# Kernel tuning notes

Hardware: AMD Instinct MI355X
Metric: run time of the kernel (lower is better)

Reference implementation:

```python
import jax, jax.numpy as jnp
import numpy as np

N_BUCKETS = 512
SLOTS_PER_BUCKET = 32
TAU = 0.1
ALPHA = 0.5


def _l2norm(x, eps=1e-12):
    return x / jnp.maximum(jnp.linalg.norm(x, axis=-1, keepdims=True), eps)


def setup_inputs() -> dict:
    key = jax.random.key(0)
    ks = jax.random.split(key, 6)
    B, T, D = 2, 2048, 1024
    total_slots = N_BUCKETS * SLOTS_PER_BUCKET
    vocab = 50257
    query_emb = jax.random.normal(ks[0], (B, T, D), dtype=jnp.float32)
    tids = jax.random.randint(ks[1], (B, T), 0, vocab)
    slot_keys = jax.random.normal(ks[2], (total_slots, D), dtype=jnp.float32)
    slot_values = jax.random.normal(ks[3], (total_slots, D), dtype=jnp.float32)
    slot_tids = jax.random.randint(ks[4], (total_slots,), 0, vocab)
    centroid_codebook = _l2norm(jax.random.normal(ks[5], (N_BUCKETS, D), dtype=jnp.float32))
    return {
        "query_emb": query_emb,
        "tids": tids,
        "slot_keys": slot_keys,
        "slot_values": slot_values,
        "slot_tids": slot_tids,
        "centroid_codebook": centroid_codebook,
    }


def reference(query_emb, tids, slot_keys, slot_values, slot_tids, centroid_codebook):
    # CentroidAddressableManifold.read
    buckets = tids % N_BUCKETS                                  # [B,T]
    lex_anchors = centroid_codebook[buckets]                    # [B,T,D]
    q_norm = _l2norm(query_emb)
    # bucket-indexed gather of 32 slots per token
    indices = buckets[..., None] * SLOTS_PER_BUCKET + jnp.arange(SLOTS_PER_BUCKET)  # [B,T,S]
    b_keys = slot_keys[indices]                                 # [B,T,S,D]
    b_vals = slot_values[indices]                               # [B,T,S,D]
    unified_query = _l2norm(ALPHA * q_norm + (1.0 - ALPHA) * lex_anchors)
    scores = jnp.einsum("btd,btsd->bts", unified_query, b_keys)  # [B,T,S]
    # hard-match path
    gathered_tids = slot_tids[indices]                          # [B,T,S]
    match_mask = (tids[..., None] == gathered_tids).astype(scores.dtype)
    match_sum = match_mask.sum(axis=-1, keepdims=True)
    has_match = match_sum > 0
    probs_hard = match_mask / (match_sum + 1e-9)
    probs_soft = jax.nn.softmax(scores / TAU, axis=-1)
    val_hard = jnp.einsum("bts,btsw->btw", probs_hard, b_vals)
    val_soft = jnp.einsum("bts,btsw->btw", probs_soft, b_vals)
    val_out = jnp.where(has_match, val_hard, val_soft)          # [B,T,D]
    return val_out
```

## Files before the change

### kernel.cpp

```cpp
#include <hip/hip_runtime.h>

#define NB 512
#define SLOTS 32
#define D 1024
#define D4 256
#define TC 8
#define CAP 64
#define TAU_INV 10.0f
#define BT 256

__global__ void k_zero(int* __restrict__ cnt) {
    if (threadIdx.x < NB) cnt[threadIdx.x] = 0;
}

__global__ void k_build(const int* __restrict__ tids, int n,
                        int* __restrict__ cnt, int* __restrict__ list) {
    int i = blockIdx.x * 256 + threadIdx.x;
    if (i < n) {
        int b = tids[i] & (NB - 1);
        int p = atomicAdd(&cnt[b], 1);
        if (p < CAP) list[b * CAP + p] = i;
    }
}

__global__ __launch_bounds__(BT, 2)
void k_main(const float* __restrict__ query,
            const int*   __restrict__ tids,
            const float* __restrict__ skeys,
            const float* __restrict__ svals,
            const int*   __restrict__ stids,
            const float* __restrict__ centroid,
            float*       __restrict__ out,
            const int*   __restrict__ cnt,
            const int*   __restrict__ list)
{
    const int bucket = blockIdx.x & (NB - 1);
    const int part   = blockIdx.x >> 9;
    const int tidx   = threadIdx.x;
    const int lane   = tidx & 63;
    const int wid    = tidx >> 6;

    const int count = min(cnt[bucket], CAP);
    const int ncnt  = (count - part + 1) >> 1;
    if (ncnt <= 0) return;

    __shared__ float s_uq[TC][D];
    __shared__ float s_scores[TC][SLOTS];
    __shared__ float s_probs[TC][SLOTS];
    __shared__ int   s_tok[TC];
    __shared__ int   s_ttid[TC];

    const int slot_tid = stids[bucket * SLOTS + (lane & 31)];
    const float4* kb = (const float4*)(skeys + (size_t)bucket * SLOTS * D);
    const float4* vb = (const float4*)(svals + (size_t)bucket * SLOTS * D);
    const float4* cb = (const float4*)(centroid + (size_t)bucket * D);

    for (int c0 = 0; c0 < ncnt; c0 += TC) {
        const int nt = min(TC, ncnt - c0);

        for (int t = wid; t < nt; t += 4) {
            const int tok = list[bucket * CAP + part + 2 * (c0 + t)];
            const float4* q4 = (const float4*)(query + (size_t)tok * D);
            float4 qv[4], anc[4];
            float ss = 0.f;
            #pragma unroll
            for (int j = 0; j < 4; ++j) {
                qv[j]  = q4[lane + 64 * j];
                anc[j] = cb[lane + 64 * j];
                ss += qv[j].x*qv[j].x + qv[j].y*qv[j].y + qv[j].z*qv[j].z + qv[j].w*qv[j].w;
            }
            #pragma unroll
            for (int off = 32; off >= 1; off >>= 1) ss += __shfl_xor(ss, off);
            const float qn = 0.5f / fmaxf(sqrtf(ss), 1e-12f);
            float4 uv[4];
            float ss2 = 0.f;
            #pragma unroll
            for (int j = 0; j < 4; ++j) {
                uv[j].x = qv[j].x * qn + 0.5f * anc[j].x;
                uv[j].y = qv[j].y * qn + 0.5f * anc[j].y;
                uv[j].z = qv[j].z * qn + 0.5f * anc[j].z;
                uv[j].w = qv[j].w * qn + 0.5f * anc[j].w;
                ss2 += uv[j].x*uv[j].x + uv[j].y*uv[j].y + uv[j].z*uv[j].z + uv[j].w*uv[j].w;
            }
            #pragma unroll
            for (int off = 32; off >= 1; off >>= 1) ss2 += __shfl_xor(ss2, off);
            const float un = 1.0f / fmaxf(sqrtf(ss2), 1e-12f);
            #pragma unroll
            for (int j = 0; j < 4; ++j) {
                ((float4*)s_uq[t])[lane + 64 * j] =
                    make_float4(uv[j].x*un, uv[j].y*un, uv[j].z*un, uv[j].w*un);
            }
            if (lane == 0) { s_tok[t] = tok; s_ttid[t] = tids[tok]; }
        }
        __syncthreads();

        #pragma unroll 1
        for (int rnd = 0; rnd < 2; ++rnd) {
            const int sbase = rnd * 16 + wid * 4;
            const float4* kr = kb + (size_t)sbase * D4;
            float4 k0[4], k1[4], k2[4], k3[4];
            #pragma unroll
            for (int j = 0; j < 4; ++j) {
                k0[j] = kr[0 * D4 + lane + 64 * j];
                k1[j] = kr[1 * D4 + lane + 64 * j];
                k2[j] = kr[2 * D4 + lane + 64 * j];
                k3[j] = kr[3 * D4 + lane + 64 * j];
            }
            for (int t = 0; t < nt; ++t) {
                const float4* u4 = (const float4*)s_uq[t];
                float P0 = 0.f, P1 = 0.f, P2 = 0.f, P3 = 0.f;
                #pragma unroll
                for (int j = 0; j < 4; ++j) {
                    float4 u = u4[lane + 64 * j];
                    P0 += k0[j].x*u.x + k0[j].y*u.y + k0[j].z*u.z + k0[j].w*u.w;
                    P1 += k1[j].x*u.x + k1[j].y*u.y + k1[j].z*u.z + k1[j].w*u.w;
                    P2 += k2[j].x*u.x + k2[j].y*u.y + k2[j].z*u.z + k2[j].w*u.w;
                    P3 += k3[j].x*u.x + k3[j].y*u.y + k3[j].z*u.z + k3[j].w*u.w;
                }
                {
                    const bool hi = (lane & 1) != 0;
                    const float sA = hi ? P0 : P2, kA = hi ? P2 : P0;
                    P0 = kA + __shfl_xor(sA, 1);
                    const float sB = hi ? P1 : P3, kB = hi ? P3 : P1;
                    P1 = kB + __shfl_xor(sB, 1);
                }
                {
                    const bool hi = (lane & 2) != 0;
                    const float sA = hi ? P0 : P1, kA = hi ? P1 : P0;
                    P0 = kA + __shfl_xor(sA, 2);
                }
                P0 += __shfl_xor(P0, 4);
                P0 += __shfl_xor(P0, 8);
                P0 += __shfl_xor(P0, 16);
                P0 += __shfl_xor(P0, 32);
                if (lane < 4)
                    s_scores[t][sbase + (((lane & 1) << 1) | ((lane >> 1) & 1))] = P0;
            }
        }
        __syncthreads();

        for (int t = wid; t < nt; t += 4) {
            if (lane < 32) {
                const float sc = s_scores[t][lane];
                float mx = sc;
                #pragma unroll
                for (int off = 16; off >= 1; off >>= 1) mx = fmaxf(mx, __shfl_xor(mx, off));
                const float e = __expf((sc - mx) * TAU_INV);
                const float f = (slot_tid == s_ttid[t]) ? 1.f : 0.f;
                float es = e, ms = f;
                #pragma unroll
                for (int off = 16; off >= 1; off >>= 1) {
                    es += __shfl_xor(es, off);
                    ms += __shfl_xor(ms, off);
                }
                s_probs[t][lane] = (ms > 0.f) ? f / (ms + 1e-9f) : e / es;
            }
        }
        __syncthreads();

        {
            float4 acc[TC];
            #pragma unroll
            for (int t = 0; t < TC; ++t) acc[t] = make_float4(0.f, 0.f, 0.f, 0.f);

            #pragma unroll 1
            for (int s0 = 0; s0 < SLOTS; s0 += 8) {
                float4 v[8];
                #pragma unroll
                for (int i = 0; i < 8; ++i) v[i] = vb[(s0 + i) * D4 + tidx];
                #pragma unroll
                for (int t = 0; t < TC; ++t) {
                    if (t < nt) {
                        const float4 pA = ((const float4*)s_probs[t])[(s0 >> 2) + 0];
                        const float4 pB = ((const float4*)s_probs[t])[(s0 >> 2) + 1];
                        acc[t].x += pA.x*v[0].x + pA.y*v[1].x + pA.z*v[2].x + pA.w*v[3].x
                                  + pB.x*v[4].x + pB.y*v[5].x + pB.z*v[6].x + pB.w*v[7].x;
                        acc[t].y += pA.x*v[0].y + pA.y*v[1].y + pA.z*v[2].y + pA.w*v[3].y
                                  + pB.x*v[4].y + pB.y*v[5].y + pB.z*v[6].y + pB.w*v[7].y;
                        acc[t].z += pA.x*v[0].z + pA.y*v[1].z + pA.z*v[2].z + pA.w*v[3].z
                                  + pB.x*v[4].z + pB.y*v[5].z + pB.z*v[6].z + pB.w*v[7].z;
                        acc[t].w += pA.x*v[0].w + pA.y*v[1].w + pA.z*v[2].w + pA.w*v[3].w
                                  + pB.x*v[4].w + pB.y*v[5].w + pB.z*v[6].w + pB.w*v[7].w;
                    }
                }
            }
            #pragma unroll
            for (int t = 0; t < TC; ++t) {
                if (t < nt) {
                    ((float4*)(out + (size_t)s_tok[t] * D))[tidx] = acc[t];
                }
            }
        }
        __syncthreads();
    }
}

extern "C" void kernel_launch(void* const* d_in, const int* in_sizes, int n_in,
                              void* d_out, int out_size, void* d_ws, size_t ws_size,
                              hipStream_t stream) {
    const float* query    = (const float*)d_in[0];
    const int*   tids     = (const int*)  d_in[1];
    const float* skeys    = (const float*)d_in[2];
    const float* svals    = (const float*)d_in[3];
    const int*   stids    = (const int*)  d_in[4];
    const float* centroid = (const float*)d_in[5];
    float* out = (float*)d_out;
    const int n_tokens = in_sizes[1];

    int* cnt  = (int*)d_ws;
    int* list = cnt + NB;

    k_zero<<<1, 512, 0, stream>>>(cnt);
    k_build<<<(n_tokens + 255) / 256, 256, 0, stream>>>(tids, n_tokens, cnt, list);
    k_main<<<NB * 2, BT, 0, stream>>>(query, tids, skeys, svals, stids,
                                      centroid, out, cnt, list);
}
```

Before: 55.65 us.

## Process one token per wavefront end-to-end without shared memory or block barriers

The block-wide staging (shared unified query, scores and probs, with several __syncthreads per chunk of 8 tokens) is replaced by one token per wavefront. Each wavefront computes its normalized query, all 32 scores, the softmax and match probabilities, and the weighted value sum in registers. Probabilities move between lanes by shuffles, and the block grows to 512 threads (8 waves). This removes barriers and LDS traffic, but each wave now re-reads all 32 keys and values of the bucket per token instead of sharing them across 8 tokens, relying on L2/L1 for reuse.

```diff
diff --git a/kernel.cpp b/kernel.cpp
--- a/kernel.cpp
+++ b/kernel.cpp
@@ -4,10 +4,9 @@
 #define SLOTS 32
 #define D 1024
 #define D4 256
-#define TC 8
 #define CAP 64
 #define TAU_INV 10.0f
-#define BT 256
+#define BT 512
 
 __global__ void k_zero(int* __restrict__ cnt) {
     if (threadIdx.x < NB) cnt[threadIdx.x] = 0;
@@ -36,68 +35,64 @@
 {
     const int bucket = blockIdx.x & (NB - 1);
     const int part   = blockIdx.x >> 9;
-    const int tidx   = threadIdx.x;
-    const int lane   = tidx & 63;
-    const int wid    = tidx >> 6;
+    const int lane   = threadIdx.x & 63;
+    const int wid    = threadIdx.x >> 6;
 
     const int count = min(cnt[bucket], CAP);
     const int ncnt  = (count - part + 1) >> 1;
     if (ncnt <= 0) return;
 
-    __shared__ float s_uq[TC][D];
-    __shared__ float s_scores[TC][SLOTS];
-    __shared__ float s_probs[TC][SLOTS];
-    __shared__ int   s_tok[TC];
-    __shared__ int   s_ttid[TC];
-
-    const int slot_tid = stids[bucket * SLOTS + (lane & 31)];
+    const int ls      = lane & 31;
+    const int my_slot = (ls & ~3) | (((ls & 1) << 1) | ((ls >> 1) & 1));
+    const int my_stid = stids[bucket * SLOTS + my_slot];
+
     const float4* kb = (const float4*)(skeys + (size_t)bucket * SLOTS * D);
     const float4* vb = (const float4*)(svals + (size_t)bucket * SLOTS * D);
     const float4* cb = (const float4*)(centroid + (size_t)bucket * D);
 
-    for (int c0 = 0; c0 < ncnt; c0 += TC) {
-        const int nt = min(TC, ncnt - c0);
-
-        for (int t = wid; t < nt; t += 4) {
-            const int tok = list[bucket * CAP + part + 2 * (c0 + t)];
+    float4 anc[4];
+    #pragma unroll
+    for (int j = 0; j < 4; ++j) anc[j] = cb[lane + 64 * j];
+
+    for (int t = wid; t < ncnt; t += 8) {
+        const int tok    = list[bucket * CAP + part + 2 * t];
+        const int my_tid = tids[tok];
+
+        float4 uq[4];
+        {
             const float4* q4 = (const float4*)(query + (size_t)tok * D);
-            float4 qv[4], anc[4];
+            float4 qv[4];
             float ss = 0.f;
             #pragma unroll
             for (int j = 0; j < 4; ++j) {
-                qv[j]  = q4[lane + 64 * j];
-                anc[j] = cb[lane + 64 * j];
+                qv[j] = q4[lane + 64 * j];
                 ss += qv[j].x*qv[j].x + qv[j].y*qv[j].y + qv[j].z*qv[j].z + qv[j].w*qv[j].w;
             }
             #pragma unroll
             for (int off = 32; off >= 1; off >>= 1) ss += __shfl_xor(ss, off);
             const float qn = 0.5f / fmaxf(sqrtf(ss), 1e-12f);
-            float4 uv[4];
             float ss2 = 0.f;
             #pragma unroll
             for (int j = 0; j < 4; ++j) {
-                uv[j].x = qv[j].x * qn + 0.5f * anc[j].x;
-                uv[j].y = qv[j].y * qn + 0.5f * anc[j].y;
-                uv[j].z = qv[j].z * qn + 0.5f * anc[j].z;
-                uv[j].w = qv[j].w * qn + 0.5f * anc[j].w;
-                ss2 += uv[j].x*uv[j].x + uv[j].y*uv[j].y + uv[j].z*uv[j].z + uv[j].w*uv[j].w;
+                uq[j].x = qv[j].x * qn + 0.5f * anc[j].x;
+                uq[j].y = qv[j].y * qn + 0.5f * anc[j].y;
+                uq[j].z = qv[j].z * qn + 0.5f * anc[j].z;
+                uq[j].w = qv[j].w * qn + 0.5f * anc[j].w;
+                ss2 += uq[j].x*uq[j].x + uq[j].y*uq[j].y + uq[j].z*uq[j].z + uq[j].w*uq[j].w;
             }
             #pragma unroll
             for (int off = 32; off >= 1; off >>= 1) ss2 += __shfl_xor(ss2, off);
             const float un = 1.0f / fmaxf(sqrtf(ss2), 1e-12f);
             #pragma unroll
             for (int j = 0; j < 4; ++j) {
-                ((float4*)s_uq[t])[lane + 64 * j] =
-                    make_float4(uv[j].x*un, uv[j].y*un, uv[j].z*un, uv[j].w*un);
-            }
-            if (lane == 0) { s_tok[t] = tok; s_ttid[t] = tids[tok]; }
-        }
-        __syncthreads();
-
+                uq[j].x *= un; uq[j].y *= un; uq[j].z *= un; uq[j].w *= un;
+            }
+        }
+
+        float sc = 0.f;
         #pragma unroll 1
-        for (int rnd = 0; rnd < 2; ++rnd) {
-            const int sbase = rnd * 16 + wid * 4;
-            const float4* kr = kb + (size_t)sbase * D4;
+        for (int g = 0; g < 8; ++g) {
+            const float4* kr = kb + (size_t)(g * 4) * D4;
             float4 k0[4], k1[4], k2[4], k3[4];
             #pragma unroll
             for (int j = 0; j < 4; ++j) {
@@ -106,92 +101,80 @@
                 k2[j] = kr[2 * D4 + lane + 64 * j];
                 k3[j] = kr[3 * D4 + lane + 64 * j];
             }
-            for (int t = 0; t < nt; ++t) {
-                const float4* u4 = (const float4*)s_uq[t];
-                float P0 = 0.f, P1 = 0.f, P2 = 0.f, P3 = 0.f;
-                #pragma unroll
-                for (int j = 0; j < 4; ++j) {
-                    float4 u = u4[lane + 64 * j];
-                    P0 += k0[j].x*u.x + k0[j].y*u.y + k0[j].z*u.z + k0[j].w*u.w;
-                    P1 += k1[j].x*u.x + k1[j].y*u.y + k1[j].z*u.z + k1[j].w*u.w;
-                    P2 += k2[j].x*u.x + k2[j].y*u.y + k2[j].z*u.z + k2[j].w*u.w;
-                    P3 += k3[j].x*u.x + k3[j].y*u.y + k3[j].z*u.z + k3[j].w*u.w;
-                }
-                {
-                    const bool hi = (lane & 1) != 0;
-                    const float sA = hi ? P0 : P2, kA = hi ? P2 : P0;
-                    P0 = kA + __shfl_xor(sA, 1);
-                    const float sB = hi ? P1 : P3, kB = hi ? P3 : P1;
-                    P1 = kB + __shfl_xor(sB, 1);
-                }
-                {
-                    const bool hi = (lane & 2) != 0;
-                    const float sA = hi ? P0 : P1, kA = hi ? P1 : P0;
-                    P0 = kA + __shfl_xor(sA, 2);
-                }
-                P0 += __shfl_xor(P0, 4);
-                P0 += __shfl_xor(P0, 8);
-                P0 += __shfl_xor(P0, 16);
-                P0 += __shfl_xor(P0, 32);
-                if (lane < 4)
-                    s_scores[t][sbase + (((lane & 1) << 1) | ((lane >> 1) & 1))] = P0;
-            }
-        }
-        __syncthreads();
-
-        for (int t = wid; t < nt; t += 4) {
-            if (lane < 32) {
-                const float sc = s_scores[t][lane];
-                float mx = sc;
-                #pragma unroll
-                for (int off = 16; off >= 1; off >>= 1) mx = fmaxf(mx, __shfl_xor(mx, off));
-                const float e = __expf((sc - mx) * TAU_INV);
-                const float f = (slot_tid == s_ttid[t]) ? 1.f : 0.f;
-                float es = e, ms = f;
-                #pragma unroll
-                for (int off = 16; off >= 1; off >>= 1) {
-                    es += __shfl_xor(es, off);
-                    ms += __shfl_xor(ms, off);
-                }
-                s_probs[t][lane] = (ms > 0.f) ? f / (ms + 1e-9f) : e / es;
-            }
-        }
-        __syncthreads();
-
+            float P0 = 0.f, P1 = 0.f, P2 = 0.f, P3 = 0.f;
+            #pragma unroll
+            for (int j = 0; j < 4; ++j) {
+                const float4 u = uq[j];
+                P0 += k0[j].x*u.x + k0[j].y*u.y + k0[j].z*u.z + k0[j].w*u.w;
+                P1 += k1[j].x*u.x + k1[j].y*u.y + k1[j].z*u.z + k1[j].w*u.w;
+                P2 += k2[j].x*u.x + k2[j].y*u.y + k2[j].z*u.z + k2[j].w*u.w;
+                P3 += k3[j].x*u.x + k3[j].y*u.y + k3[j].z*u.z + k3[j].w*u.w;
+            }
+            {
+                const bool hi = (lane & 1) != 0;
+                const float sA = hi ? P0 : P2, kA = hi ? P2 : P0;
+                P0 = kA + __shfl_xor(sA, 1);
+                const float sB = hi ? P1 : P3, kB = hi ? P3 : P1;
+                P1 = kB + __shfl_xor(sB, 1);
+            }
+            {
+                const bool hi = (lane & 2) != 0;
+                const float sA = hi ? P0 : P1, kA = hi ? P1 : P0;
+                P0 = kA + __shfl_xor(sA, 2);
+            }
+            P0 += __shfl_xor(P0, 4);
+            P0 += __shfl_xor(P0, 8);
+            P0 += __shfl_xor(P0, 16);
+            P0 += __shfl_xor(P0, 32);
+            if ((ls >> 2) == g) sc = P0;
+        }
+
+        float p;
         {
-            float4 acc[TC];
-            #pragma unroll
-            for (int t = 0; t < TC; ++t) acc[t] = make_float4(0.f, 0.f, 0.f, 0.f);
-
-            #pragma unroll 1
-            for (int s0 = 0; s0 < SLOTS; s0 += 8) {
-                float4 v[8];
-                #pragma unroll
-                for (int i = 0; i < 8; ++i) v[i] = vb[(s0 + i) * D4 + tidx];
-                #pragma unroll
-                for (int t = 0; t < TC; ++t) {
-                    if (t < nt) {
-                        const float4 pA = ((const float4*)s_probs[t])[(s0 >> 2) + 0];
-                        const float4 pB = ((const float4*)s_probs[t])[(s0 >> 2) + 1];
-                        acc[t].x += pA.x*v[0].x + pA.y*v[1].x + pA.z*v[2].x + pA.w*v[3].x
-                                  + pB.x*v[4].x + pB.y*v[5].x + pB.z*v[6].x + pB.w*v[7].x;
-                        acc[t].y += pA.x*v[0].y + pA.y*v[1].y + pA.z*v[2].y + pA.w*v[3].y
-                                  + pB.x*v[4].y + pB.y*v[5].y + pB.z*v[6].y + pB.w*v[7].y;
-                        acc[t].z += pA.x*v[0].z + pA.y*v[1].z + pA.z*v[2].z + pA.w*v[3].z
-                                  + pB.x*v[4].z + pB.y*v[5].z + pB.z*v[6].z + pB.w*v[7].z;
-                        acc[t].w += pA.x*v[0].w + pA.y*v[1].w + pA.z*v[2].w + pA.w*v[3].w
-                                  + pB.x*v[4].w + pB.y*v[5].w + pB.z*v[6].w + pB.w*v[7].w;
-                    }
-                }
-            }
-            #pragma unroll
-            for (int t = 0; t < TC; ++t) {
-                if (t < nt) {
-                    ((float4*)(out + (size_t)s_tok[t] * D))[tidx] = acc[t];
-                }
-            }
-        }
-        __syncthreads();
+            float m = sc;
+            #pragma unroll
+            for (int off = 16; off >= 1; off >>= 1) m = fmaxf(m, __shfl_xor(m, off));
+            const float e = __expf((sc - m) * TAU_INV);
+            const float f = (my_stid == my_tid) ? 1.f : 0.f;
+            float es = e, ms = f;
+            #pragma unroll
+            for (int off = 16; off >= 1; off >>= 1) {
+                es += __shfl_xor(es, off);
+                ms += __shfl_xor(ms, off);
+            }
+            p = (ms > 0.f) ? f / (ms + 1e-9f) : e / es;
+        }
+
+        float4 acc[4];
+        #pragma unroll
+        for (int j = 0; j < 4; ++j) acc[j] = make_float4(0.f, 0.f, 0.f, 0.f);
+        #pragma unroll 1
+        for (int g = 0; g < 8; ++g) {
+            const float4* vr = vb + (size_t)(g * 4) * D4;
+            float4 r0[4], r1[4], r2[4], r3[4];
+            #pragma unroll
+            for (int j = 0; j < 4; ++j) {
+                r0[j] = vr[0 * D4 + lane + 64 * j];
+                r1[j] = vr[1 * D4 + lane + 64 * j];
+                r2[j] = vr[2 * D4 + lane + 64 * j];
+                r3[j] = vr[3 * D4 + lane + 64 * j];
+            }
+            const float ws0 = __shfl(p, g * 4 + 0);
+            const float ws1 = __shfl(p, g * 4 + 2);
+            const float ws2 = __shfl(p, g * 4 + 1);
+            const float ws3 = __shfl(p, g * 4 + 3);
+            #pragma unroll
+            for (int j = 0; j < 4; ++j) {
+                acc[j].x += ws0*r0[j].x + ws1*r1[j].x + ws2*r2[j].x + ws3*r3[j].x;
+                acc[j].y += ws0*r0[j].y + ws1*r1[j].y + ws2*r2[j].y + ws3*r3[j].y;
+                acc[j].z += ws0*r0[j].z + ws1*r1[j].z + ws2*r2[j].z + ws3*r3[j].z;
+                acc[j].w += ws0*r0[j].w + ws1*r1[j].w + ws2*r2[j].w + ws3*r3[j].w;
+            }
+        }
+
+        float4* o4 = (float4*)(out + (size_t)tok * D);
+        #pragma unroll
+        for (int j = 0; j < 4; ++j) o4[lane + 64 * j] = acc[j];
     }
 }
 
```

Result: slower. 72.79 us (+30.8%).

## Split buckets four ways and give each wave one token for value reduction

Applied to the files above, without the earlier changes.

Each bucket's token list is now split across four blocks instead of two, with a token chunk of four, so every wave owns exactly one token. Each wave computes its own softmax/hard-match probabilities and then reduces all 32 value rows for that token itself, broadcasting the weights with shuffles. This removes the shared probability buffer, one barrier, and the shared token/tid arrays. In exchange, each wave rereads all value rows on its own rather than the block sharing them across tokens, and each block covers fewer tokens, so the block launches more work for less reuse of keys and values.

```diff
diff --git a/kernel.cpp b/kernel.cpp
--- a/kernel.cpp
+++ b/kernel.cpp
@@ -4,7 +4,7 @@
 #define SLOTS 32
 #define D 1024
 #define D4 256
-#define TC 8
+#define TC 4
 #define CAP 64
 #define TAU_INV 10.0f
 #define BT 256
@@ -35,22 +35,20 @@
             const int*   __restrict__ list)
 {
     const int bucket = blockIdx.x & (NB - 1);
-    const int part   = blockIdx.x >> 9;
+    const int q      = blockIdx.x >> 9;
     const int tidx   = threadIdx.x;
     const int lane   = tidx & 63;
     const int wid    = tidx >> 6;
+    const int ls     = lane & 31;
 
     const int count = min(cnt[bucket], CAP);
-    const int ncnt  = (count - part + 1) >> 1;
+    const int ncnt  = (count - q + 3) >> 2;
     if (ncnt <= 0) return;
 
     __shared__ float s_uq[TC][D];
     __shared__ float s_scores[TC][SLOTS];
-    __shared__ float s_probs[TC][SLOTS];
-    __shared__ int   s_tok[TC];
-    __shared__ int   s_ttid[TC];
-
-    const int slot_tid = stids[bucket * SLOTS + (lane & 31)];
+
+    const int slot_tid = stids[bucket * SLOTS + ls];
     const float4* kb = (const float4*)(skeys + (size_t)bucket * SLOTS * D);
     const float4* vb = (const float4*)(svals + (size_t)bucket * SLOTS * D);
     const float4* cb = (const float4*)(centroid + (size_t)bucket * D);
@@ -58,8 +56,10 @@
     for (int c0 = 0; c0 < ncnt; c0 += TC) {
         const int nt = min(TC, ncnt - c0);
 
-        for (int t = wid; t < nt; t += 4) {
-            const int tok = list[bucket * CAP + part + 2 * (c0 + t)];
+        int tok = -1, my_tid = 0;
+        if (wid < nt) {
+            tok = list[bucket * CAP + q + 4 * (c0 + wid)];
+            my_tid = tids[tok];
             const float4* q4 = (const float4*)(query + (size_t)tok * D);
             float4 qv[4], anc[4];
             float ss = 0.f;
@@ -87,10 +87,9 @@
             const float un = 1.0f / fmaxf(sqrtf(ss2), 1e-12f);
             #pragma unroll
             for (int j = 0; j < 4; ++j) {
-                ((float4*)s_uq[t])[lane + 64 * j] =
+                ((float4*)s_uq[wid])[lane + 64 * j] =
                     make_float4(uv[j].x*un, uv[j].y*un, uv[j].z*un, uv[j].w*un);
             }
-            if (lane == 0) { s_tok[t] = tok; s_ttid[t] = tids[tok]; }
         }
         __syncthreads();
 
@@ -139,59 +138,52 @@
         }
         __syncthreads();
 
-        for (int t = wid; t < nt; t += 4) {
-            if (lane < 32) {
-                const float sc = s_scores[t][lane];
-                float mx = sc;
+        if (wid < nt) {
+            const float sc = s_scores[wid][ls];
+            float mx = sc;
+            #pragma unroll
+            for (int off = 16; off >= 1; off >>= 1) mx = fmaxf(mx, __shfl_xor(mx, off));
+            const float e = __expf((sc - mx) * TAU_INV);
+            const float f = (slot_tid == my_tid) ? 1.f : 0.f;
+            float es = e, ms = f;
+            #pragma unroll
+            for (int off = 16; off >= 1; off >>= 1) {
+                es += __shfl_xor(es, off);
+                ms += __shfl_xor(ms, off);
+            }
+            const float p = (ms > 0.f) ? f / (ms + 1e-9f) : e / es;
+
+            float4 acc[4];
+            #pragma unroll
+            for (int j = 0; j < 4; ++j) acc[j] = make_float4(0.f, 0.f, 0.f, 0.f);
+            #pragma unroll 1
+            for (int g = 0; g < 8; ++g) {
+                const float4* vr = vb + (size_t)(g * 4) * D4;
+                float4 r0[4], r1[4], r2[4], r3[4];
                 #pragma unroll
-                for (int off = 16; off >= 1; off >>= 1) mx = fmaxf(mx, __shfl_xor(mx, off));
-                const float e = __expf((sc - mx) * TAU_INV);
-                const float f = (slot_tid == s_ttid[t]) ? 1.f : 0.f;
-                float es = e, ms = f;
+                for (int j = 0; j < 4; ++j) {
+                    r0[j] = vr[0 * D4 + lane + 64 * j];
+                    r1[j] = vr[1 * D4 + lane + 64 * j];
+                    r2[j] = vr[2 * D4 + lane + 64 * j];
+                    r3[j] = vr[3 * D4 + lane + 64 * j];
+                }
+                const float w0 = __shfl(p, g * 4 + 0);
+                const float w1 = __shfl(p, g * 4 + 1);
+                const float w2 = __shfl(p, g * 4 + 2);
+                const float w3 = __shfl(p, g * 4 + 3);
                 #pragma unroll
-                for (int off = 16; off >= 1; off >>= 1) {
-                    es += __shfl_xor(es, off);
-                    ms += __shfl_xor(ms, off);
-                }
-                s_probs[t][lane] = (ms > 0.f) ? f / (ms + 1e-9f) : e / es;
-            }
+                for (int j = 0; j < 4; ++j) {
+                    acc[j].x += w0*r0[j].x + w1*r1[j].x + w2*r2[j].x + w3*r3[j].x;
+                    acc[j].y += w0*r0[j].y + w1*r1[j].y + w2*r2[j].y + w3*r3[j].y;
+                    acc[j].z += w0*r0[j].z + w1*r1[j].z + w2*r2[j].z + w3*r3[j].z;
+                    acc[j].w += w0*r0[j].w + w1*r1[j].w + w2*r2[j].w + w3*r3[j].w;
+                }
+            }
+            float4* o4 = (float4*)(out + (size_t)tok * D);
+            #pragma unroll
+            for (int j = 0; j < 4; ++j) o4[lane + 64 * j] = acc[j];
         }
-        __syncthreads();
-
-        {
-            float4 acc[TC];
-            #pragma unroll
-            for (int t = 0; t < TC; ++t) acc[t] = make_float4(0.f, 0.f, 0.f, 0.f);
-
-            #pragma unroll 1
-            for (int s0 = 0; s0 < SLOTS; s0 += 8) {
-                float4 v[8];
-                #pragma unroll
-                for (int i = 0; i < 8; ++i) v[i] = vb[(s0 + i) * D4 + tidx];
-                #pragma unroll
-                for (int t = 0; t < TC; ++t) {
-                    if (t < nt) {
-                        const float4 pA = ((const float4*)s_probs[t])[(s0 >> 2) + 0];
-                        const float4 pB = ((const float4*)s_probs[t])[(s0 >> 2) + 1];
-                        acc[t].x += pA.x*v[0].x + pA.y*v[1].x + pA.z*v[2].x + pA.w*v[3].x
-                                  + pB.x*v[4].x + pB.y*v[5].x + pB.z*v[6].x + pB.w*v[7].x;
-                        acc[t].y += pA.x*v[0].y + pA.y*v[1].y + pA.z*v[2].y + pA.w*v[3].y
-                                  + pB.x*v[4].y + pB.y*v[5].y + pB.z*v[6].y + pB.w*v[7].y;
-                        acc[t].z += pA.x*v[0].z + pA.y*v[1].z + pA.z*v[2].z + pA.w*v[3].z
-                                  + pB.x*v[4].z + pB.y*v[5].z + pB.z*v[6].z + pB.w*v[7].z;
-                        acc[t].w += pA.x*v[0].w + pA.y*v[1].w + pA.z*v[2].w + pA.w*v[3].w
-                                  + pB.x*v[4].w + pB.y*v[5].w + pB.z*v[6].w + pB.w*v[7].w;
-                    }
-                }
-            }
-            #pragma unroll
-            for (int t = 0; t < TC; ++t) {
-                if (t < nt) {
-                    ((float4*)(out + (size_t)s_tok[t] * D))[tidx] = acc[t];
-                }
-            }
-        }
-        __syncthreads();
+        if (c0 + TC < ncnt) __syncthreads();
     }
 }
 
@@ -212,6 +204,6 @@
 
     k_zero<<<1, 512, 0, stream>>>(cnt);
     k_build<<<(n_tokens + 255) / 256, 256, 0, stream>>>(tids, n_tokens, cnt, list);
-    k_main<<<NB * 2, BT, 0, stream>>>(query, tids, skeys, svals, stids,
+    k_main<<<NB * 4, BT, 0, stream>>>(query, tids, skeys, svals, stids,
                                       centroid, out, cnt, list);
 }
```

New measurement: 95.31 us. +71.3%, slower.

## Split unified-query normalization into a separate kernel staged through the output buffer

Applied to the files above, without the earlier changes.

Moves the per-token query/anchor blend and L2 normalization out of the bucket kernel into a new kernel with one wavefront per token. That kernel writes the normalized query into the output buffer, and the main kernel reads it back from global memory instead of shared memory, then overwrites the same row with the result. This drops 32 KB of LDS per block and the per-bucket serial normalization phase, which should help occupancy and load balance. The cost is an extra launch and an extra global write and read of a full activation-sized tensor. The trailing barrier is also skipped on the last chunk.

```diff
diff --git a/kernel.cpp b/kernel.cpp
--- a/kernel.cpp
+++ b/kernel.cpp
@@ -24,13 +24,58 @@
 }
 
 __global__ __launch_bounds__(BT, 2)
-void k_main(const float* __restrict__ query,
-            const int*   __restrict__ tids,
+void k_uq(const float* __restrict__ query,
+          const int*   __restrict__ tids,
+          const float* __restrict__ centroid,
+          float*       __restrict__ uq_out,
+          int n_tokens)
+{
+    const int lane = threadIdx.x & 63;
+    const int wid  = threadIdx.x >> 6;
+    const int tok  = blockIdx.x * 4 + wid;
+    if (tok >= n_tokens) return;
+
+    const int b = tids[tok] & (NB - 1);
+    const float4* q4 = (const float4*)(query + (size_t)tok * D);
+    const float4* cb = (const float4*)(centroid + (size_t)b * D);
+
+    float4 qv[4], anc[4];
+    float ss = 0.f;
+    #pragma unroll
+    for (int j = 0; j < 4; ++j) {
+        qv[j]  = q4[lane + 64 * j];
+        anc[j] = cb[lane + 64 * j];
+        ss += qv[j].x*qv[j].x + qv[j].y*qv[j].y + qv[j].z*qv[j].z + qv[j].w*qv[j].w;
+    }
+    #pragma unroll
+    for (int off = 32; off >= 1; off >>= 1) ss += __shfl_xor(ss, off);
+    const float qn = 0.5f / fmaxf(sqrtf(ss), 1e-12f);
+    float4 uv[4];
+    float ss2 = 0.f;
+    #pragma unroll
+    for (int j = 0; j < 4; ++j) {
+        uv[j].x = qv[j].x * qn + 0.5f * anc[j].x;
+        uv[j].y = qv[j].y * qn + 0.5f * anc[j].y;
+        uv[j].z = qv[j].z * qn + 0.5f * anc[j].z;
+        uv[j].w = qv[j].w * qn + 0.5f * anc[j].w;
+        ss2 += uv[j].x*uv[j].x + uv[j].y*uv[j].y + uv[j].z*uv[j].z + uv[j].w*uv[j].w;
+    }
+    #pragma unroll
+    for (int off = 32; off >= 1; off >>= 1) ss2 += __shfl_xor(ss2, off);
+    const float un = 1.0f / fmaxf(sqrtf(ss2), 1e-12f);
+    float4* o4 = (float4*)(uq_out + (size_t)tok * D);
+    #pragma unroll
+    for (int j = 0; j < 4; ++j)
+        o4[lane + 64 * j] = make_float4(uv[j].x*un, uv[j].y*un, uv[j].z*un, uv[j].w*un);
+}
+
+__global__ __launch_bounds__(BT, 2)
+void k_main(const int*   __restrict__ tids,
+            const float*              uq,
             const float* __restrict__ skeys,
             const float* __restrict__ svals,
             const int*   __restrict__ stids,
-            const float* __restrict__ centroid,
-            float*       __restrict__ out,
+            float*                    out,
             const int*   __restrict__ cnt,
             const int*   __restrict__ list)
 {
@@ -44,7 +89,6 @@
     const int ncnt  = (count - part + 1) >> 1;
     if (ncnt <= 0) return;
 
-    __shared__ float s_uq[TC][D];
     __shared__ float s_scores[TC][SLOTS];
     __shared__ float s_probs[TC][SLOTS];
     __shared__ int   s_tok[TC];
@@ -53,44 +97,14 @@
     const int slot_tid = stids[bucket * SLOTS + (lane & 31)];
     const float4* kb = (const float4*)(skeys + (size_t)bucket * SLOTS * D);
     const float4* vb = (const float4*)(svals + (size_t)bucket * SLOTS * D);
-    const float4* cb = (const float4*)(centroid + (size_t)bucket * D);
 
     for (int c0 = 0; c0 < ncnt; c0 += TC) {
         const int nt = min(TC, ncnt - c0);
 
-        for (int t = wid; t < nt; t += 4) {
-            const int tok = list[bucket * CAP + part + 2 * (c0 + t)];
-            const float4* q4 = (const float4*)(query + (size_t)tok * D);
-            float4 qv[4], anc[4];
-            float ss = 0.f;
-            #pragma unroll
-            for (int j = 0; j < 4; ++j) {
-                qv[j]  = q4[lane + 64 * j];
-                anc[j] = cb[lane + 64 * j];
-                ss += qv[j].x*qv[j].x + qv[j].y*qv[j].y + qv[j].z*qv[j].z + qv[j].w*qv[j].w;
-            }
-            #pragma unroll
-            for (int off = 32; off >= 1; off >>= 1) ss += __shfl_xor(ss, off);
-            const float qn = 0.5f / fmaxf(sqrtf(ss), 1e-12f);
-            float4 uv[4];
-            float ss2 = 0.f;
-            #pragma unroll
-            for (int j = 0; j < 4; ++j) {
-                uv[j].x = qv[j].x * qn + 0.5f * anc[j].x;
-                uv[j].y = qv[j].y * qn + 0.5f * anc[j].y;
-                uv[j].z = qv[j].z * qn + 0.5f * anc[j].z;
-                uv[j].w = qv[j].w * qn + 0.5f * anc[j].w;
-                ss2 += uv[j].x*uv[j].x + uv[j].y*uv[j].y + uv[j].z*uv[j].z + uv[j].w*uv[j].w;
-            }
-            #pragma unroll
-            for (int off = 32; off >= 1; off >>= 1) ss2 += __shfl_xor(ss2, off);
-            const float un = 1.0f / fmaxf(sqrtf(ss2), 1e-12f);
-            #pragma unroll
-            for (int j = 0; j < 4; ++j) {
-                ((float4*)s_uq[t])[lane + 64 * j] =
-                    make_float4(uv[j].x*un, uv[j].y*un, uv[j].z*un, uv[j].w*un);
-            }
-            if (lane == 0) { s_tok[t] = tok; s_ttid[t] = tids[tok]; }
+        if (tidx < nt) {
+            const int tok = list[bucket * CAP + part + 2 * (c0 + tidx)];
+            s_tok[tidx]  = tok;
+            s_ttid[tidx] = tids[tok];
         }
         __syncthreads();
 
@@ -107,7 +121,7 @@
                 k3[j] = kr[3 * D4 + lane + 64 * j];
             }
             for (int t = 0; t < nt; ++t) {
-                const float4* u4 = (const float4*)s_uq[t];
+                const float4* u4 = (const float4*)(uq + (size_t)s_tok[t] * D);
                 float P0 = 0.f, P1 = 0.f, P2 = 0.f, P3 = 0.f;
                 #pragma unroll
                 for (int j = 0; j < 4; ++j) {
@@ -191,7 +205,7 @@
                 }
             }
         }
-        __syncthreads();
+        if (c0 + TC < ncnt) __syncthreads();
     }
 }
 
@@ -212,6 +226,7 @@
 
     k_zero<<<1, 512, 0, stream>>>(cnt);
     k_build<<<(n_tokens + 255) / 256, 256, 0, stream>>>(tids, n_tokens, cnt, list);
-    k_main<<<NB * 2, BT, 0, stream>>>(query, tids, skeys, svals, stids,
-                                      centroid, out, cnt, list);
-}
+    k_uq<<<(n_tokens + 3) / 4, BT, 0, stream>>>(query, tids, centroid, out, n_tokens);
+    k_main<<<NB * 2, BT, 0, stream>>>(tids, out, skeys, svals, stids,
+                                      out, cnt, list);
+}
```

Measured after the change: 66.18 us. 18.9% more time.
